# Kernel tuning notes

Hardware: AMD Instinct MI355X
Metric: run time of the kernel (lower is better)

The kernel has to match this reference:

```python
import jax, jax.numpy as jnp
import numpy as np

BOX = 120          # box_size
RES = 1.0          # resolution (also Gaussian sigma)
NTYPES = 11        # num_atom_types (hard-coded in module)
D = 2              # splat half-width in cells -> (2D+1)^3 = 125 voxels/atom
B = 4
NATOMS = 2200      # 200 atoms per type


def setup_inputs() -> dict:
    key = jax.random.key(0)
    # atoms uniformly inside the box interior so splats mostly land in-bounds
    coords = jax.random.uniform(key, (B, NATOMS * 3), dtype=jnp.float32,
                                minval=20.0, maxval=100.0)
    per_type = NATOMS // NTYPES
    num_atoms_of_type = jnp.full((B, NTYPES), per_type, dtype=jnp.int32)
    offsets = jnp.tile(jnp.arange(NTYPES, dtype=jnp.int32) * per_type, (B, 1))
    return {"input_coords": coords,
            "num_atoms_of_type": num_atoms_of_type,
            "offsets": offsets}


def _splat(coords, num_atoms_of_type, offsets):
    # coords: [B, N, 3]; per-atom Gaussian splat into typed volume
    Bn, N, _ = coords.shape
    atom_idx = jnp.arange(N)

    def per_batch_types(off, num):
        # atoms [off[t], off[t]+num[t]) belong to type t
        t = jnp.clip(jnp.searchsorted(off, atom_idx, side='right') - 1, 0, NTYPES - 1)
        valid = (atom_idx >= off[t]) & (atom_idx < off[t] + num[t])
        return t, valid

    types, valid = jax.vmap(per_batch_types)(offsets, num_atoms_of_type)  # [B,N]

    # (2D+1)^3 window of integer cell offsets
    w = jnp.arange(-D, D + 1)
    wx, wy, wz = jnp.meshgrid(w, w, w, indexing='ij')
    win = jnp.stack([wx.ravel(), wy.ravel(), wz.ravel()], axis=-1)  # [W,3]

    base = jnp.floor(coords / RES).astype(jnp.int32)                 # [B,N,3]
    cells = base[:, :, None, :] + win[None, None, :, :]              # [B,N,W,3]
    centers = cells.astype(coords.dtype) * RES                       # voxel coords
    r2 = jnp.sum((centers - coords[:, :, None, :]) ** 2, axis=-1)    # [B,N,W]
    vals = jnp.exp(-r2 / (RES * RES))                                # Gaussian density

    inb = jnp.all((cells >= 0) & (cells < BOX), axis=-1)             # [B,N,W]
    ok = inb & valid[:, :, None]
    flat = (types[:, :, None] * (BOX * BOX * BOX)
            + cells[..., 0] * (BOX * BOX) + cells[..., 1] * BOX + cells[..., 2])
    flat = jnp.where(ok, flat, NTYPES * BOX * BOX * BOX)  # out-of-range -> dropped
    vals = jnp.where(ok, vals, jnp.zeros_like(vals))

    def scatter(f, v):
        vol = jnp.zeros((NTYPES * BOX * BOX * BOX,), dtype=coords.dtype)
        return vol.at[f.ravel()].add(v.ravel(), mode='drop')

    vol = jax.vmap(scatter)(flat, vals)
    return vol.reshape(Bn, NTYPES, BOX, BOX, BOX)


def reference(input_coords, num_atoms_of_type, offsets):
    coords = input_coords.reshape(input_coords.shape[0], -1, 3)
    return _splat(coords, num_atoms_of_type, offsets)
```

## Files before the change

kernel.cpp:

```cpp
#include <hip/hip_runtime.h>


#define BOX    120
#define NTYPES 11
#define DHALF  2
#define WIN    5
#define WVOX   125
#define BOX3   (BOX * BOX * BOX)

__global__ void zero_kernel(float* __restrict__ out, long long n) {
    long long n4 = n >> 2;
    float4* out4 = reinterpret_cast<float4*>(out);
    long long i = (long long)blockIdx.x * blockDim.x + threadIdx.x;
    long long stride = (long long)gridDim.x * blockDim.x;
    float4 z = make_float4(0.f, 0.f, 0.f, 0.f);
    for (; i < n4; i += stride) out4[i] = z;
    if (blockIdx.x == 0) {
        long long tail_start = n4 << 2;
        long long t = tail_start + threadIdx.x;
        if (t < n) out[t] = 0.f;
    }
}

__global__ void splat_kernel(const float* __restrict__ coords,
                             const int*  __restrict__ num_atoms_of_type,
                             const int*  __restrict__ offsets,
                             float* __restrict__ out,
                             int batch, int natoms) {
    int gid  = blockIdx.x * blockDim.x + threadIdx.x;
    int atom = gid >> 7;
    int j    = gid & 127;
    if (atom >= batch * natoms || j >= WVOX) return;

    int b = atom / natoms;
    int i = atom - b * natoms;

    const float* c = coords + ((long long)b * natoms + i) * 3;
    float x = c[0], y = c[1], z = c[2];

    const int* off = offsets          + b * NTYPES;
    const int* num = num_atoms_of_type + b * NTYPES;

    int t = 0;
#pragma unroll
    for (int k = 1; k < NTYPES; ++k) {
        if (off[k] <= i) t = k;
    }
    bool valid = (i >= off[t]) && (i < off[t] + num[t]);
    if (!valid) return;

    int bx = (int)floorf(x);
    int by = (int)floorf(y);
    int bz = (int)floorf(z);

    int wx = j / 25;
    int rem = j - wx * 25;
    int wy = rem / 5;
    int wz = rem - wy * 5;

    int cx = bx + wx - DHALF;
    int cy = by + wy - DHALF;
    int cz = bz + wz - DHALF;
    if ((unsigned)cx >= (unsigned)BOX ||
        (unsigned)cy >= (unsigned)BOX ||
        (unsigned)cz >= (unsigned)BOX) return;

    float dx = (float)cx - x;
    float dy = (float)cy - y;
    float dz = (float)cz - z;
    float r2 = dx * dx + dy * dy + dz * dz;
    float val = expf(-r2);

    int idx = (b * NTYPES + t) * BOX3 + cx * (BOX * BOX) + cy * BOX + cz;
    atomicAdd(&out[idx], val);
}

extern "C" void kernel_launch(void* const* d_in, const int* in_sizes, int n_in,
                              void* d_out, int out_size, void* d_ws, size_t ws_size,
                              hipStream_t stream) {
    const float* coords = (const float*)d_in[0];
    const int*   num    = (const int*)d_in[1];
    const int*   off    = (const int*)d_in[2];
    float*       out    = (float*)d_out;

    int batch  = in_sizes[1] / NTYPES;
    int natoms = in_sizes[0] / (3 * batch);

    zero_kernel<<<8192, 256, 0, stream>>>(out, (long long)out_size);

    int total_threads = batch * natoms * 128;
    int blocks = (total_threads + 255) / 256;
    splat_kernel<<<blocks, 256, 0, stream>>>(coords, num, off, out,
                                             batch, natoms);
}
```

Before: 323.3 us.

## Replace atomic scatter splat with spatial binning and per-voxel gather

Atoms are first binned into a 2D grid of 4x4-cell columns per batch. A gather kernel then has each thread own one voxel column position and accumulate all 11 type densities from nearby bins in registers, writing each output element exactly once. This removes the separate full-volume zeroing pass and the tens of millions of scattered float atomics. The trade-offs are a fixed bin capacity of 64, which silently drops atoms if a bin overflows, per-thread loops over neighbouring atom lists with divergent filtering, and use of workspace memory.

Measured after the change: 367.2 us. +13.6%, slower.

```diff
diff --git a/kernel.cpp b/kernel.cpp
--- a/kernel.cpp
+++ b/kernel.cpp
@@ -4,75 +4,108 @@
 #define BOX    120
 #define NTYPES 11
 #define DHALF  2
-#define WIN    5
-#define WVOX   125
 #define BOX3   (BOX * BOX * BOX)
 
-__global__ void zero_kernel(float* __restrict__ out, long long n) {
-    long long n4 = n >> 2;
-    float4* out4 = reinterpret_cast<float4*>(out);
-    long long i = (long long)blockIdx.x * blockDim.x + threadIdx.x;
-    long long stride = (long long)gridDim.x * blockDim.x;
-    float4 z = make_float4(0.f, 0.f, 0.f, 0.f);
-    for (; i < n4; i += stride) out4[i] = z;
-    if (blockIdx.x == 0) {
-        long long tail_start = n4 << 2;
-        long long t = tail_start + threadIdx.x;
-        if (t < n) out[t] = 0.f;
-    }
+#define BINSZ   4
+#define NBIN    30
+#define NBIN2   (NBIN * NBIN)
+#define CAP     64
+
+__global__ void zero_counts_kernel(int* __restrict__ counts, int n) {
+    int i = blockIdx.x * blockDim.x + threadIdx.x;
+    if (i < n) counts[i] = 0;
 }
 
-__global__ void splat_kernel(const float* __restrict__ coords,
-                             const int*  __restrict__ num_atoms_of_type,
-                             const int*  __restrict__ offsets,
-                             float* __restrict__ out,
-                             int batch, int natoms) {
-    int gid  = blockIdx.x * blockDim.x + threadIdx.x;
-    int atom = gid >> 7;
-    int j    = gid & 127;
-    if (atom >= batch * natoms || j >= WVOX) return;
-
-    int b = atom / natoms;
-    int i = atom - b * natoms;
+__global__ void bin_kernel(const float* __restrict__ coords,
+                           const int*  __restrict__ num_atoms_of_type,
+                           const int*  __restrict__ offsets,
+                           float4* __restrict__ bins,
+                           int*    __restrict__ counts,
+                           int batch, int natoms) {
+    int gid = blockIdx.x * blockDim.x + threadIdx.x;
+    if (gid >= batch * natoms) return;
+    int b = gid / natoms;
+    int i = gid - b * natoms;
 
     const float* c = coords + ((long long)b * natoms + i) * 3;
     float x = c[0], y = c[1], z = c[2];
 
-    const int* off = offsets          + b * NTYPES;
+    const int* off = offsets           + b * NTYPES;
     const int* num = num_atoms_of_type + b * NTYPES;
 
     int t = 0;
 #pragma unroll
-    for (int k = 1; k < NTYPES; ++k) {
+    for (int k = 1; k < NTYPES; ++k)
         if (off[k] <= i) t = k;
-    }
-    bool valid = (i >= off[t]) && (i < off[t] + num[t]);
-    if (!valid) return;
+    if (!(i >= off[t] && i < off[t] + num[t])) return;
 
     int bx = (int)floorf(x);
     int by = (int)floorf(y);
     int bz = (int)floorf(z);
+    if (bx < -DHALF || bx >= BOX + DHALF ||
+        by < -DHALF || by >= BOX + DHALF ||
+        bz < -DHALF || bz >= BOX + DHALF) return;
 
-    int wx = j / 25;
-    int rem = j - wx * 25;
-    int wy = rem / 5;
-    int wz = rem - wy * 5;
+    int cbx = min(BOX - 1, max(0, bx)) / BINSZ;
+    int cby = min(BOX - 1, max(0, by)) / BINSZ;
+    int bin = b * NBIN2 + cbx * NBIN + cby;
 
-    int cx = bx + wx - DHALF;
-    int cy = by + wy - DHALF;
-    int cz = bz + wz - DHALF;
-    if ((unsigned)cx >= (unsigned)BOX ||
-        (unsigned)cy >= (unsigned)BOX ||
-        (unsigned)cz >= (unsigned)BOX) return;
+    int slot = atomicAdd(&counts[bin], 1);
+    if (slot < CAP)
+        bins[(long long)bin * CAP + slot] =
+            make_float4(x, y, z, __int_as_float(t));
+}
 
-    float dx = (float)cx - x;
-    float dy = (float)cy - y;
-    float dz = (float)cz - z;
-    float r2 = dx * dx + dy * dy + dz * dz;
-    float val = expf(-r2);
+__global__ void gather_kernel(const float4* __restrict__ bins,
+                              const int*    __restrict__ counts,
+                              float* __restrict__ out) {
+    int bid = blockIdx.x;
+    int y = bid % BOX; bid /= BOX;
+    int x = bid % BOX; bid /= BOX;
+    int b = bid;
+    int z = threadIdx.x;
+    bool zon = (z < BOX);
 
-    int idx = (b * NTYPES + t) * BOX3 + cx * (BOX * BOX) + cy * BOX + cz;
-    atomicAdd(&out[idx], val);
+    float acc[NTYPES];
+#pragma unroll
+    for (int k = 0; k < NTYPES; ++k) acc[k] = 0.f;
+
+    int bx0 = max(0, x - DHALF) / BINSZ;
+    int bx1 = min(BOX - 1, x + DHALF) / BINSZ;
+    int by0 = max(0, y - DHALF) / BINSZ;
+    int by1 = min(BOX - 1, y + DHALF) / BINSZ;
+
+    for (int cbx = bx0; cbx <= bx1; ++cbx) {
+        for (int cby = by0; cby <= by1; ++cby) {
+            int bin = b * NBIN2 + cbx * NBIN + cby;
+            int cnt = min(counts[bin], CAP);
+            const float4* lst = bins + (long long)bin * CAP;
+            for (int j = 0; j < cnt; ++j) {
+                float4 a = lst[j];
+                int abx = (int)floorf(a.x);
+                int aby = (int)floorf(a.y);
+                int abz = (int)floorf(a.z);
+                if (abs(x - abx) > DHALF || abs(y - aby) > DHALF) continue;
+                bool hit = zon && (abs(z - abz) <= DHALF);
+                float dx = (float)x - a.x;
+                float dy = (float)y - a.y;
+                float dz = (float)z - a.z;
+                float r2 = dx * dx + dy * dy + dz * dz;
+                float val = hit ? expf(-r2) : 0.f;
+                int t = __float_as_int(a.w);
+#pragma unroll
+                for (int k = 0; k < NTYPES; ++k)
+                    acc[k] += (t == k) ? val : 0.f;
+            }
+        }
+    }
+
+    if (zon) {
+        int base = x * (BOX * BOX) + y * BOX + z;
+#pragma unroll
+        for (int k = 0; k < NTYPES; ++k)
+            out[(long long)(b * NTYPES + k) * BOX3 + base] = acc[k];
+    }
 }
 
 extern "C" void kernel_launch(void* const* d_in, const int* in_sizes, int n_in,
@@ -86,10 +119,16 @@
     int batch  = in_sizes[1] / NTYPES;
     int natoms = in_sizes[0] / (3 * batch);
 
-    zero_kernel<<<8192, 256, 0, stream>>>(out, (long long)out_size);
+    int    nbins  = batch * NBIN2;
+    int*   counts = (int*)d_ws;
+    size_t bins_off = ((size_t)nbins * sizeof(int) + 15) & ~(size_t)15;
+    float4* bins  = (float4*)((char*)d_ws + bins_off);
 
-    int total_threads = batch * natoms * 128;
-    int blocks = (total_threads + 255) / 256;
-    splat_kernel<<<blocks, 256, 0, stream>>>(coords, num, off, out,
-                                             batch, natoms);
+    zero_counts_kernel<<<(nbins + 255) / 256, 256, 0, stream>>>(counts, nbins);
+
+    int natom_threads = batch * natoms;
+    bin_kernel<<<(natom_threads + 255) / 256, 256, 0, stream>>>(
+        coords, num, off, bins, counts, batch, natoms);
+
+    gather_kernel<<<batch * BOX * BOX, 128, 0, stream>>>(bins, counts, out);
 }
```
